# Optimization experiments

Hardware: AMD Instinct MI355X
Metric: run time of the kernel (lower is better)

The kernel has to match this reference:

```python
import jax, jax.numpy as jnp
import numpy as np

B, S, D_IN = 4, 2048, 1024
D_OUT, H = 1024, 16
HD = D_OUT // H  # head_dim = 64

def setup_inputs() -> dict:
    key = jax.random.key(0)
    ks = jax.random.split(key, 6)
    scale_in = 1.0 / np.sqrt(D_IN)
    scale_out = 1.0 / np.sqrt(D_OUT)
    return {
        "x": jax.random.normal(ks[0], (B, S, D_IN), dtype=jnp.float32),
        "Wq": jax.random.uniform(ks[1], (D_OUT, D_IN), jnp.float32, -scale_in, scale_in),
        "Wk": jax.random.uniform(ks[2], (D_OUT, D_IN), jnp.float32, -scale_in, scale_in),
        "Wv": jax.random.uniform(ks[3], (D_OUT, D_IN), jnp.float32, -scale_in, scale_in),
        "Wo": jax.random.uniform(ks[4], (D_OUT, D_OUT), jnp.float32, -scale_out, scale_out),
        "bo": jax.random.uniform(ks[5], (D_OUT,), jnp.float32, -scale_out, scale_out),
    }

def reference(x, Wq, Wk, Wv, Wo, bo):
    b, s, _ = x.shape
    # projections (nn.Linear: x @ W.T), split into heads -> [b, h, s, hd]
    def proj(W):
        return jnp.einsum('bsd,ed->bse', x, W).reshape(b, s, H, HD).transpose(0, 2, 1, 3)
    q, k, v = proj(Wq), proj(Wk), proj(Wv)
    # full score matrix [b, h, s, s] with causal mask, scaled softmax
    scores = jnp.einsum('bhqd,bhkd->bhqk', q, k)
    causal = jnp.tril(jnp.ones((s, s), dtype=bool))
    scores = jnp.where(causal, scores, -jnp.inf)
    attn = jax.nn.softmax(scores / np.sqrt(HD), axis=-1)
    # dropout p=0.0 -> identity
    ctx = jnp.einsum('bhqk,bhkd->bqhd', attn, v).reshape(b, s, D_OUT)
    return jnp.einsum('bsd,ed->bse', ctx, Wo) + bo
```

## Files before the change

### kernel.cpp

```cpp
#include <hip/hip_runtime.h>
#include <cstdint>
#include <cstddef>

#define S_LEN   2048
#define D_MODEL 1024
#define N_HEADS 16
#define HEAD_DIM 64
#define BATCH   4
#define M_ROWS  (BATCH * S_LEN)

typedef _Float16 half8  __attribute__((ext_vector_type(8)));
typedef _Float16 half4v __attribute__((ext_vector_type(4)));
typedef float    float4v __attribute__((ext_vector_type(4)));

#define AS1 __attribute__((address_space(1)))
#define AS3 __attribute__((address_space(3)))

#define QSCL 0.1803368801111832f

__device__ __forceinline__ int swz(int row, int byteInRow) {
    return row * 128 + ((((byteInRow >> 4) ^ (row & 7)) << 4)) + (byteInRow & 15);
}

__device__ __forceinline__ int vperm(int a) {
    return (a & 0x20) | ((a & 0x0C) << 1) | ((a & 0x10) >> 2) | (a & 3);
}

__device__ __forceinline__ const half8* gfrag(const _Float16* base, int row, int q) {
    int macro = row >> 1;
    int sb = (((row & 1) << 2) | q) ^ (macro & 7);
    return (const half8*)((const char*)base + macro * 128 + sb * 16);
}
__device__ __forceinline__ size_t gsrc(int d, int K) {
    int macro = d >> 7;
    int sb = (d >> 4) & 7;
    int b = sb ^ (macro & 7);
    int r = (macro << 1) | (b >> 2);
    int cblk = b & 3;
    return (size_t)r * K + cblk * 8;
}

__global__ __launch_bounds__(256) void cvt_all(const float* __restrict__ x,
                                               const float* __restrict__ wq,
                                               const float* __restrict__ wk,
                                               const float* __restrict__ wv,
                                               const float* __restrict__ wo,
                                               _Float16* __restrict__ dst) {
    const int NX = M_ROWS * D_MODEL / 4;
    const int NW = D_MODEL * D_MODEL / 4;
    int i = blockIdx.x * 256 + threadIdx.x;
    int j = i;
    const float4v* src;
    if (j < NX) src = (const float4v*)x;
    else {
        j -= NX;
        if (j < NW) src = (const float4v*)wq;
        else { j -= NW;
            if (j < NW) src = (const float4v*)wk;
            else { j -= NW;
                if (j < NW) src = (const float4v*)wv;
                else { j -= NW; src = (const float4v*)wo; }
            }
        }
    }
    float4v v = src[j];
    half4v h;
    h[0] = (_Float16)v[0]; h[1] = (_Float16)v[1];
    h[2] = (_Float16)v[2]; h[3] = (_Float16)v[3];
    ((half4v*)dst)[i] = h;
}

template <int MODE>
__global__ __launch_bounds__(256) void gemm_bt(const _Float16* __restrict__ A,
                                               const _Float16* __restrict__ Bw,
                                               _Float16* __restrict__ O1,
                                               _Float16* __restrict__ O2,
                                               float* __restrict__ Of,
                                               const float* __restrict__ bias,
                                               int M, int N, int K) {
    __shared__ __align__(16) _Float16 As[2][128 * 32];
    __shared__ __align__(16) _Float16 Bs[2][128 * 32];

    const int tid  = threadIdx.x;
    const int wave = tid >> 6;
    const int lane = tid & 63;
    const int quad = lane >> 4;
    const int l16  = lane & 15;

    const int rowBase = blockIdx.x * 128;
    const int colBase = blockIdx.y * 128;
    const int rowOff  = (wave >> 1) * 64;
    const int colOff  = (wave & 1) * 64;

    float4v acc[4][4] = {};

    const size_t off0 = gsrc(tid * 16, K);
    const size_t off1 = gsrc(4096 + tid * 16, K);

    const _Float16* aSrc0 = A + (size_t)rowBase * K + off0;
    const _Float16* aSrc1 = A + (size_t)rowBase * K + off1;
    const _Float16* bSrc0 = Bw + (size_t)colBase * K + off0;
    const _Float16* bSrc1 = Bw + (size_t)colBase * K + off1;

    auto stage = [&](int k0, int buf) {
        __builtin_amdgcn_global_load_lds((const AS1 void*)(aSrc0 + k0),
            (AS3 void*)(As[buf] + wave * 512), 16, 0, 0);
        __builtin_amdgcn_global_load_lds((const AS1 void*)(aSrc1 + k0),
            (AS3 void*)(As[buf] + 2048 + wave * 512), 16, 0, 0);
        __builtin_amdgcn_global_load_lds((const AS1 void*)(bSrc0 + k0),
            (AS3 void*)(Bs[buf] + wave * 512), 16, 0, 0);
        __builtin_amdgcn_global_load_lds((const AS1 void*)(bSrc1 + k0),
            (AS3 void*)(Bs[buf] + 2048 + wave * 512), 16, 0, 0);
    };

    const int niter = K >> 5;
    stage(0, 0);
    for (int it = 0; it < niter; ++it) {
        __syncthreads();
        if (it + 1 < niter) stage((it + 1) << 5, (it + 1) & 1);

        const _Float16* Ab = As[it & 1];
        const _Float16* Bb = Bs[it & 1];

        half8 af[4], bf[4];
#pragma unroll
        for (int mi = 0; mi < 4; ++mi)
            af[mi] = *gfrag(Ab, rowOff + mi * 16 + l16, quad);
#pragma unroll
        for (int ni = 0; ni < 4; ++ni)
            bf[ni] = *gfrag(Bb, colOff + ni * 16 + l16, quad);

#pragma unroll
        for (int mi = 0; mi < 4; ++mi)
#pragma unroll
            for (int ni = 0; ni < 4; ++ni)
                acc[mi][ni] = __builtin_amdgcn_mfma_f32_16x16x32_f16(
                    af[mi], bf[ni], acc[mi][ni], 0, 0, 0);
    }

#pragma unroll
    for (int mi = 0; mi < 4; ++mi)
#pragma unroll
        for (int ni = 0; ni < 4; ++ni) {
            const int col = colBase + colOff + ni * 16 + l16;
#pragma unroll
            for (int i = 0; i < 4; ++i) {
                const int row = rowBase + rowOff + mi * 16 + quad * 4 + i;
                float v = acc[mi][ni][i];
                if (MODE == 0) {
                    int b_ = row >> 11, s_ = row & 2047;
                    int proj = col >> 10, d = col & 1023;
                    int h_ = d >> 6, hd = d & 63;
                    _Float16* dst = proj ? O2 : O1;
                    if (proj == 0) v *= QSCL;
                    dst[(((size_t)(b_ * 16 + h_) * 2048 + s_) << 6) + hd] = (_Float16)v;
                } else if (MODE == 1) {
                    int h_ = row >> 6, hd = row & 63;
                    int b_ = col >> 11, s_ = col & 2047;
                    int sp = (s_ & ~63) | vperm(s_ & 63);
                    O1[(((size_t)(b_ * 16 + h_) * 64 + hd) << 11) + sp] = (_Float16)v;
                } else {
                    Of[(size_t)row * N + col] = v + bias[col];
                }
            }
        }
}

template <bool MASKED>
__device__ __forceinline__ void attn_step5(const half8 qf[2],
                                           const _Float16* __restrict__ Ks,
                                           const _Float16* __restrict__ Vs,
                                           int krow0, int qt, int quad, int c,
                                           float4v o[4], float& l) {
    float4v sT[4] = {};
#pragma unroll
    for (int nt = 0; nt < 4; ++nt)
#pragma unroll
        for (int ks = 0; ks < 2; ++ks) {
            half8 kf = *(const half8*)((const char*)Ks + swz(nt * 16 + c, ks * 64 + quad * 16));
            sT[nt] = __builtin_amdgcn_mfma_f32_16x16x32_f16(kf, qf[ks], sT[nt], 0, 0, 0);
        }

    const int qrow_g = qt + c;
#pragma unroll
    for (int kk = 0; kk < 2; ++kk) {
        float e[2][4];
#pragma unroll
        for (int jh = 0; jh < 2; ++jh) {
            const int nt = 2 * kk + jh;
#pragma unroll
            for (int i = 0; i < 4; ++i) {
                float ev = __builtin_amdgcn_exp2f(sT[nt][i]);
                if (MASKED)
                    ev = (krow0 + nt * 16 + quad * 4 + i <= qrow_g) ? ev : 0.0f;
                e[jh][i] = ev;
                l += ev;
            }
        }
        auto p0 = __builtin_amdgcn_cvt_pkrtz(e[0][0], e[0][1]);
        auto p1 = __builtin_amdgcn_cvt_pkrtz(e[0][2], e[0][3]);
        auto p2 = __builtin_amdgcn_cvt_pkrtz(e[1][0], e[1][1]);
        auto p3 = __builtin_amdgcn_cvt_pkrtz(e[1][2], e[1][3]);
        half8 pf;
        pf[0] = p0[0]; pf[1] = p0[1]; pf[2] = p1[0]; pf[3] = p1[1];
        pf[4] = p2[0]; pf[5] = p2[1]; pf[6] = p3[0]; pf[7] = p3[1];
#pragma unroll
        for (int dt = 0; dt < 4; ++dt) {
            half8 vf = *(const half8*)((const char*)Vs + swz(dt * 16 + c, kk * 64 + quad * 16));
            o[dt] = __builtin_amdgcn_mfma_f32_16x16x32_f16(pf, vf, o[dt], 0, 0, 0);
        }
    }
}

__global__ __launch_bounds__(256, 4) void attn_flash5(const _Float16* __restrict__ Q,
                                                      const _Float16* __restrict__ Kg,
                                                      const _Float16* __restrict__ Vt,
                                                      _Float16* __restrict__ Ctx) {
    __shared__ __align__(16) _Float16 Ks[2 * 64 * 64];
    __shared__ __align__(16) _Float16 Vs[2 * 64 * 64];

    const int tid  = threadIdx.x;
    const int wave = tid >> 6;
    const int lane = tid & 63;
    const int quad = lane >> 4;
    const int c    = lane & 15;

    const int h    = blockIdx.x;
    const int hp   = blockIdx.y;
    const int bb   = blockIdx.z;
    const int pair = hp >> 1;
    const int hf   = hp & 1;

    const int qA = pair * 128 + hf * 64 + wave * 16;
    const int qB = (15 - pair) * 128 + hf * 64 + wave * 16;
    const int nkbB = (15 - pair) * 2 + hf + 1;

    const _Float16* Qb  = Q  + ((size_t)(bb * 16 + h) << 17);
    const _Float16* Kb  = Kg + ((size_t)(bb * 16 + h) << 17);
    const _Float16* Vtb = Vt + ((size_t)(bb * 16 + h) << 17);

    half8 qfA[2], qfB[2];
    {
        const _Float16* qa = Qb + (size_t)(qA + c) * 64;
        qfA[0] = *(const half8*)(qa + quad * 8);
        qfA[1] = *(const half8*)(qa + 32 + quad * 8);
        const _Float16* qb = Qb + (size_t)(qB + c) * 64;
        qfB[0] = *(const half8*)(qb + quad * 8);
        qfB[1] = *(const half8*)(qb + 32 + quad * 8);
    }

    size_t koff[2], voff[2];
#pragma unroll
    for (int it = 0; it < 2; ++it) {
        int F = it * 4096 + tid * 16;
        int r = F >> 7;
        int blk = (tid & 7) ^ (r & 7);
        koff[it] = (size_t)r * 64 + blk * 8;
        voff[it] = (size_t)r * 2048 + blk * 8;
    }

    float4v oA[4] = {}, oB[4] = {};
    float lA = 0.0f, lB = 0.0f;

    auto stage = [&](int kb, int buf) {
        const size_t kbase = (size_t)kb * 64 * 64;
#pragma unroll
        for (int it = 0; it < 2; ++it) {
            __builtin_amdgcn_global_load_lds(
                (const AS1 void*)(Kb + kbase + koff[it]),
                (AS3 void*)((char*)Ks + buf * 8192 + it * 4096 + wave * 1024), 16, 0, 0);
            __builtin_amdgcn_global_load_lds(
                (const AS1 void*)(Vtb + kb * 64 + voff[it]),
                (AS3 void*)((char*)Vs + buf * 8192 + it * 4096 + wave * 1024), 16, 0, 0);
        }
    };

    stage(0, 0);
    for (int kb = 0; kb < nkbB; ++kb) {
        __syncthreads();
        if (kb + 1 < nkbB) stage(kb + 1, (kb + 1) & 1);

        const _Float16* Ksb = Ks + (kb & 1) * 4096;
        const _Float16* Vsb = Vs + (kb & 1) * 4096;
        const int krow0 = kb * 64;

        if (krow0 <= qB + 15) {
            if (krow0 + 63 <= qB)
                attn_step5<false>(qfB, Ksb, Vsb, krow0, qB, quad, c, oB, lB);
            else
                attn_step5<true >(qfB, Ksb, Vsb, krow0, qB, quad, c, oB, lB);
        }
        if (krow0 <= qA + 15) {
            if (krow0 + 63 <= qA)
                attn_step5<false>(qfA, Ksb, Vsb, krow0, qA, quad, c, oA, lA);
            else
                attn_step5<true >(qfA, Ksb, Vsb, krow0, qA, quad, c, oA, lA);
        }
    }

    lA += __shfl_xor(lA, 16); lA += __shfl_xor(lA, 32);
    lB += __shfl_xor(lB, 16); lB += __shfl_xor(lB, 32);

#pragma unroll
    for (int t = 0; t < 2; ++t) {
        const float lv = t ? lB : lA;
        float4v* o = t ? oB : oA;
        const int qt = t ? qB : qA;
#pragma unroll
        for (int i = 0; i < 4; ++i) {
            const float inv = 1.0f / __shfl(lv, quad * 4 + i);
            const int row_g = qt + quad * 4 + i;
            _Float16* dst = Ctx + (size_t)(bb * 2048 + row_g) * 1024 + h * 64;
#pragma unroll
            for (int dt = 0; dt < 4; ++dt)
                dst[dt * 16 + c] = (_Float16)(o[dt][i] * inv);
        }
    }
}

extern "C" void kernel_launch(void* const* d_in, const int* in_sizes, int n_in,
                              void* d_out, int out_size, void* d_ws, size_t ws_size,
                              hipStream_t stream) {
    const float* x  = (const float*)d_in[0];
    const float* Wq = (const float*)d_in[1];
    const float* Wk = (const float*)d_in[2];
    const float* Wv = (const float*)d_in[3];
    const float* Wo = (const float*)d_in[4];
    const float* bo = (const float*)d_in[5];
    float* out = (float*)d_out;

    _Float16* Xh   = (_Float16*)d_ws;
    _Float16* Wqkh = Xh + (size_t)M_ROWS * D_MODEL;
    _Float16* Wvh  = Wqkh + (size_t)2 * D_MODEL * D_MODEL;
    _Float16* Woh  = Wvh + (size_t)D_MODEL * D_MODEL;
    _Float16* Qh   = Woh + (size_t)D_MODEL * D_MODEL;
    _Float16* Kh   = Qh + (size_t)M_ROWS * D_MODEL;
    _Float16* Vth  = Kh + (size_t)M_ROWS * D_MODEL;
    _Float16* Ch   = Vth + (size_t)M_ROWS * D_MODEL;

    const int TOT4 = (M_ROWS * D_MODEL + 4 * D_MODEL * D_MODEL) / 4;
    cvt_all<<<TOT4 / 256, 256, 0, stream>>>(x, Wq, Wk, Wv, Wo, Xh);

    gemm_bt<0><<<dim3(M_ROWS / 128, 2048 / 128), 256, 0, stream>>>(
        Xh, Wqkh, Qh, Kh, nullptr, nullptr, M_ROWS, 2048, D_MODEL);
    gemm_bt<1><<<dim3(D_MODEL / 128, M_ROWS / 128), 256, 0, stream>>>(
        Wvh, Xh, Vth, nullptr, nullptr, nullptr, D_MODEL, M_ROWS, D_MODEL);

    attn_flash5<<<dim3(N_HEADS, 16, BATCH), 256, 0, stream>>>(Qh, Kh, Vth, Ch);

    gemm_bt<2><<<dim3(M_ROWS / 128, D_MODEL / 128), 256, 0, stream>>>(
        Ch, Woh, nullptr, nullptr, out, bo, M_ROWS, D_MODEL, D_MODEL);
}
```

Baseline: 179.0 us.

## Rewrite projection GEMMs as 8-wave 256x128 triple-buffered pipelined kernel

Replaces the 4-wave 128x128 double-buffered GEMM with an 8-wave 256x128 tile kernel. It uses a 3-stage LDS ring (144KB dynamic shared memory) with K-step 64, split staging, and explicit vmcnt/lgkmcnt waits with raw s_barrier so loads stay in flight across iterations. MFMA blocks are wrapped in s_setprio raises, in both the GEMM and the attention kernel. K is hardcoded to 1024 and the large LDS footprint limits occupancy, while the epilogue's row/column offsets now come from the 2x4 wave grid.

Result: faster. 153.8 us (-14.0%).

```diff
diff --git a/kernel.cpp b/kernel.cpp
--- a/kernel.cpp
+++ b/kernel.cpp
@@ -24,20 +24,6 @@
 
 __device__ __forceinline__ int vperm(int a) {
     return (a & 0x20) | ((a & 0x0C) << 1) | ((a & 0x10) >> 2) | (a & 3);
-}
-
-__device__ __forceinline__ const half8* gfrag(const _Float16* base, int row, int q) {
-    int macro = row >> 1;
-    int sb = (((row & 1) << 2) | q) ^ (macro & 7);
-    return (const half8*)((const char*)base + macro * 128 + sb * 16);
-}
-__device__ __forceinline__ size_t gsrc(int d, int K) {
-    int macro = d >> 7;
-    int sb = (d >> 4) & 7;
-    int b = sb ^ (macro & 7);
-    int r = (macro << 1) | (b >> 2);
-    int cblk = b & 3;
-    return (size_t)r * K + cblk * 8;
 }
 
 __global__ __launch_bounds__(256) void cvt_all(const float* __restrict__ x,
@@ -70,74 +56,114 @@
     ((half4v*)dst)[i] = h;
 }
 
+#define GK   1024
+#define GNT  16
+#define BUFB 49152
+#define GEMM_LDS (3 * BUFB)
+
 template <int MODE>
-__global__ __launch_bounds__(256) void gemm_bt(const _Float16* __restrict__ A,
-                                               const _Float16* __restrict__ Bw,
-                                               _Float16* __restrict__ O1,
-                                               _Float16* __restrict__ O2,
-                                               float* __restrict__ Of,
-                                               const float* __restrict__ bias,
-                                               int M, int N, int K) {
-    __shared__ __align__(16) _Float16 As[2][128 * 32];
-    __shared__ __align__(16) _Float16 Bs[2][128 * 32];
+__global__ __launch_bounds__(512, 2) void gemm8p(const _Float16* __restrict__ A,
+                                                 const _Float16* __restrict__ Bw,
+                                                 _Float16* __restrict__ O1,
+                                                 _Float16* __restrict__ O2,
+                                                 float* __restrict__ Of,
+                                                 const float* __restrict__ bias,
+                                                 int N) {
+    extern __shared__ char smem[];
 
     const int tid  = threadIdx.x;
     const int wave = tid >> 6;
     const int lane = tid & 63;
     const int quad = lane >> 4;
     const int l16  = lane & 15;
-
-    const int rowBase = blockIdx.x * 128;
+    const int wm   = wave >> 1;
+    const int wn   = wave & 1;
+
+    const int rowBase = blockIdx.x * 256;
     const int colBase = blockIdx.y * 128;
-    const int rowOff  = (wave >> 1) * 64;
-    const int colOff  = (wave & 1) * 64;
+
+    const int srow = tid >> 3;
+    const int csw  = ((tid & 7) ^ (srow & 7)) * 8;
+    const _Float16* aS[4];
+    const _Float16* bS[2];
+#pragma unroll
+    for (int i = 0; i < 4; ++i)
+        aS[i] = A + (size_t)(rowBase + i * 64 + srow) * GK + csw;
+#pragma unroll
+    for (int j = 0; j < 2; ++j)
+        bS[j] = Bw + (size_t)(colBase + j * 64 + srow) * GK + csw;
+    const int dstOff = tid * 16;
+
+    auto stage = [&](int kt, int part) {
+        char* base = smem + (kt % 3) * BUFB;
+        const size_t ko = (size_t)kt * 64;
+        if (part == 0) {
+            __builtin_amdgcn_global_load_lds((const AS1 void*)(aS[0] + ko),
+                (AS3 void*)(base + 0 * 8192 + dstOff), 16, 0, 0);
+            __builtin_amdgcn_global_load_lds((const AS1 void*)(aS[1] + ko),
+                (AS3 void*)(base + 1 * 8192 + dstOff), 16, 0, 0);
+            __builtin_amdgcn_global_load_lds((const AS1 void*)(bS[0] + ko),
+                (AS3 void*)(base + 32768 + dstOff), 16, 0, 0);
+        } else {
+            __builtin_amdgcn_global_load_lds((const AS1 void*)(aS[2] + ko),
+                (AS3 void*)(base + 2 * 8192 + dstOff), 16, 0, 0);
+            __builtin_amdgcn_global_load_lds((const AS1 void*)(aS[3] + ko),
+                (AS3 void*)(base + 3 * 8192 + dstOff), 16, 0, 0);
+            __builtin_amdgcn_global_load_lds((const AS1 void*)(bS[1] + ko),
+                (AS3 void*)(base + 32768 + 8192 + dstOff), 16, 0, 0);
+        }
+    };
+
+    const int aRow = (wm * 64 + l16) * 128;
+    const int bRow = (wn * 64 + l16) * 128;
+    int swzk[2];
+    swzk[0] = ((quad)     ^ (l16 & 7)) << 4;
+    swzk[1] = ((quad + 4) ^ (l16 & 7)) << 4;
 
     float4v acc[4][4] = {};
 
-    const size_t off0 = gsrc(tid * 16, K);
-    const size_t off1 = gsrc(4096 + tid * 16, K);
-
-    const _Float16* aSrc0 = A + (size_t)rowBase * K + off0;
-    const _Float16* aSrc1 = A + (size_t)rowBase * K + off1;
-    const _Float16* bSrc0 = Bw + (size_t)colBase * K + off0;
-    const _Float16* bSrc1 = Bw + (size_t)colBase * K + off1;
-
-    auto stage = [&](int k0, int buf) {
-        __builtin_amdgcn_global_load_lds((const AS1 void*)(aSrc0 + k0),
-            (AS3 void*)(As[buf] + wave * 512), 16, 0, 0);
-        __builtin_amdgcn_global_load_lds((const AS1 void*)(aSrc1 + k0),
-            (AS3 void*)(As[buf] + 2048 + wave * 512), 16, 0, 0);
-        __builtin_amdgcn_global_load_lds((const AS1 void*)(bSrc0 + k0),
-            (AS3 void*)(Bs[buf] + wave * 512), 16, 0, 0);
-        __builtin_amdgcn_global_load_lds((const AS1 void*)(bSrc1 + k0),
-            (AS3 void*)(Bs[buf] + 2048 + wave * 512), 16, 0, 0);
-    };
-
-    const int niter = K >> 5;
-    stage(0, 0);
-    for (int it = 0; it < niter; ++it) {
-        __syncthreads();
-        if (it + 1 < niter) stage((it + 1) << 5, (it + 1) & 1);
-
-        const _Float16* Ab = As[it & 1];
-        const _Float16* Bb = Bs[it & 1];
-
-        half8 af[4], bf[4];
-#pragma unroll
-        for (int mi = 0; mi < 4; ++mi)
-            af[mi] = *gfrag(Ab, rowOff + mi * 16 + l16, quad);
-#pragma unroll
-        for (int ni = 0; ni < 4; ++ni)
-            bf[ni] = *gfrag(Bb, colOff + ni * 16 + l16, quad);
-
-#pragma unroll
-        for (int mi = 0; mi < 4; ++mi)
+    stage(0, 0); stage(0, 1); stage(1, 0); stage(1, 1);
+    asm volatile("s_waitcnt vmcnt(6)" ::: "memory");
+    __builtin_amdgcn_s_barrier();
+
+#pragma unroll
+    for (int kt = 0; kt < GNT; ++kt) {
+        const char* Ab = smem + (kt % 3) * BUFB;
+        const char* Bb = Ab + 32768;
+#pragma unroll
+        for (int ks = 0; ks < 2; ++ks) {
+            half8 af[4], bf[4];
+#pragma unroll
+            for (int mi = 0; mi < 4; ++mi)
+                af[mi] = *(const half8*)(Ab + aRow + mi * 2048 + swzk[ks]);
 #pragma unroll
             for (int ni = 0; ni < 4; ++ni)
-                acc[mi][ni] = __builtin_amdgcn_mfma_f32_16x16x32_f16(
-                    af[mi], bf[ni], acc[mi][ni], 0, 0, 0);
-    }
-
+                bf[ni] = *(const half8*)(Bb + bRow + ni * 2048 + swzk[ks]);
+            if (kt + 2 < GNT) stage(kt + 2, ks);
+            __builtin_amdgcn_s_barrier();
+            asm volatile("s_waitcnt lgkmcnt(0)" ::: "memory");
+            __builtin_amdgcn_sched_barrier(0);
+            __builtin_amdgcn_s_setprio(1);
+#pragma unroll
+            for (int mi = 0; mi < 4; ++mi)
+#pragma unroll
+                for (int ni = 0; ni < 4; ++ni)
+                    acc[mi][ni] = __builtin_amdgcn_mfma_f32_16x16x32_f16(
+                        af[mi], bf[ni], acc[mi][ni], 0, 0, 0);
+            __builtin_amdgcn_s_setprio(0);
+            if (ks == 1) {
+                if (kt + 2 < GNT) {
+                    asm volatile("s_waitcnt vmcnt(6)" ::: "memory");
+                } else if (kt + 1 < GNT) {
+                    asm volatile("s_waitcnt vmcnt(0)" ::: "memory");
+                }
+            }
+            __builtin_amdgcn_s_barrier();
+        }
+    }
+
+    const int rowOff = wm * 64;
+    const int colOff = wn * 64;
 #pragma unroll
     for (int mi = 0; mi < 4; ++mi)
 #pragma unroll
@@ -173,6 +199,7 @@
                                            int krow0, int qt, int quad, int c,
                                            float4v o[4], float& l) {
     float4v sT[4] = {};
+    __builtin_amdgcn_s_setprio(1);
 #pragma unroll
     for (int nt = 0; nt < 4; ++nt)
 #pragma unroll
@@ -180,6 +207,7 @@
             half8 kf = *(const half8*)((const char*)Ks + swz(nt * 16 + c, ks * 64 + quad * 16));
             sT[nt] = __builtin_amdgcn_mfma_f32_16x16x32_f16(kf, qf[ks], sT[nt], 0, 0, 0);
         }
+    __builtin_amdgcn_s_setprio(0);
 
     const int qrow_g = qt + c;
 #pragma unroll
@@ -204,11 +232,13 @@
         half8 pf;
         pf[0] = p0[0]; pf[1] = p0[1]; pf[2] = p1[0]; pf[3] = p1[1];
         pf[4] = p2[0]; pf[5] = p2[1]; pf[6] = p3[0]; pf[7] = p3[1];
+        __builtin_amdgcn_s_setprio(1);
 #pragma unroll
         for (int dt = 0; dt < 4; ++dt) {
             half8 vf = *(const half8*)((const char*)Vs + swz(dt * 16 + c, kk * 64 + quad * 16));
             o[dt] = __builtin_amdgcn_mfma_f32_16x16x32_f16(pf, vf, o[dt], 0, 0, 0);
         }
+        __builtin_amdgcn_s_setprio(0);
     }
 }
 
@@ -338,16 +368,27 @@
     _Float16* Vth  = Kh + (size_t)M_ROWS * D_MODEL;
     _Float16* Ch   = Vth + (size_t)M_ROWS * D_MODEL;
 
+    static bool s_init = false;
+    if (!s_init) {
+        hipFuncSetAttribute((const void*)gemm8p<0>,
+                            hipFuncAttributeMaxDynamicSharedMemorySize, GEMM_LDS);
+        hipFuncSetAttribute((const void*)gemm8p<1>,
+                            hipFuncAttributeMaxDynamicSharedMemorySize, GEMM_LDS);
+        hipFuncSetAttribute((const void*)gemm8p<2>,
+                            hipFuncAttributeMaxDynamicSharedMemorySize, GEMM_LDS);
+        s_init = true;
+    }
+
     const int TOT4 = (M_ROWS * D_MODEL + 4 * D_MODEL * D_MODEL) / 4;
     cvt_all<<<TOT4 / 256, 256, 0, stream>>>(x, Wq, Wk, Wv, Wo, Xh);
 
-    gemm_bt<0><<<dim3(M_ROWS / 128, 2048 / 128), 256, 0, stream>>>(
-        Xh, Wqkh, Qh, Kh, nullptr, nullptr, M_ROWS, 2048, D_MODEL);
-    gemm_bt<1><<<dim3(D_MODEL / 128, M_ROWS / 128), 256, 0, stream>>>(
-        Wvh, Xh, Vth, nullptr, nullptr, nullptr, D_MODEL, M_ROWS, D_MODEL);
+    gemm8p<0><<<dim3(M_ROWS / 256, 2048 / 128), 512, GEMM_LDS, stream>>>(
+        Xh, Wqkh, Qh, Kh, nullptr, nullptr, 2048);
+    gemm8p<1><<<dim3(D_MODEL / 256, M_ROWS / 128), 512, GEMM_LDS, stream>>>(
+        Wvh, Xh, Vth, nullptr, nullptr, nullptr, M_ROWS);
 
     attn_flash5<<<dim3(N_HEADS, 16, BATCH), 256, 0, stream>>>(Qh, Kh, Vth, Ch);
 
-    gemm_bt<2><<<dim3(M_ROWS / 128, D_MODEL / 128), 256, 0, stream>>>(
-        Ch, Woh, nullptr, nullptr, out, bo, M_ROWS, D_MODEL, D_MODEL);
-}
+    gemm8p<2><<<dim3(M_ROWS / 256, D_MODEL / 128), 512, GEMM_LDS, stream>>>(
+        Ch, Woh, nullptr, nullptr, out, bo, D_MODEL);
+}
```
